# Performance work log

Hardware: AMD Instinct MI355X
Metric: run time of the kernel (lower is better)

The kernel has to match this reference:

```python
import jax, jax.numpy as jnp
import numpy as np

B, N, M = 8192, 64, 32          # batch, num_fields, embedding_dim
D = N * (N - 1) // 2            # 2016 pairwise-interaction rows of theta
OUT = 1024                      # block_out_dim
BN_EPS = 1e-5


def setup_inputs() -> dict:
    key = jax.random.key(0)
    k0, k1, k2, k3 = jax.random.split(key, 4)
    inputs = jax.random.normal(k0, (B, N * M), dtype=jnp.float32)
    W_z = jax.random.normal(k1, (N, N, M), dtype=jnp.float32) * 0.05
    theta = jax.random.normal(k2, (D, N), dtype=jnp.float32) * 0.05
    w_affine = jax.random.normal(k3, (OUT, N + D), dtype=jnp.float32) * 0.02
    b_affine = jnp.zeros((OUT,), dtype=jnp.float32)
    gamma = jnp.ones((OUT,), dtype=jnp.float32)
    beta = jnp.zeros((OUT,), dtype=jnp.float32)
    return {"inputs": inputs, "W_z": W_z, "theta": theta,
            "w_affine": w_affine, "b_affine": b_affine,
            "gamma": gamma, "beta": beta}


def reference(inputs, W_z, theta, w_affine, b_affine, gamma, beta):
    b = inputs.shape[0]
    x = inputs.reshape(b, N, M)                      # [B, N, M]
    # lz term: full quadratic form with W_z
    lz = jnp.einsum('bnm,dnm->bd', x, W_z)           # [B, N]
    # lp term: algebraically identical to einsum('bdnm,bdnm->bd') over
    # delta = einsum('bnm,dn->bdnm'): lp[b,d] = sum_n theta[d,n]^2 * sum_m x[b,n,m]^2
    x_sq = jnp.sum(x * x, axis=-1)                   # [B, N]
    lp = x_sq @ (theta * theta).T                    # [B, D]
    out = jnp.concatenate([lz, lp], axis=1)          # [B, N+D]
    out = out @ w_affine.T + b_affine                # [B, OUT]
    # BatchNorm1d in training mode (batch statistics, biased variance)
    mean = jnp.mean(out, axis=0)
    var = jnp.var(out, axis=0)
    out = (out - mean) * jax.lax.rsqrt(var + BN_EPS) * gamma + beta
    return out
```

## Files before the change

### kernel.cpp

```cpp
#include <hip/hip_runtime.h>
#include <stdint.h>

#define NROWS 8192
#define KX    2048
#define KA    2112
#define NF    64
#define DD    2016
#define WCOLS 2080
#define ODIM  1024
#define BN_EPS 1e-5f

#define A1_OT 32
#define A2_DC 8
#define A2_DPC 252
#define A2_OT 16

#define CONV_RPB 4
#define CONV_NB  (NROWS / CONV_RPB)
#define RED_NB   (ODIM * NF / 256)

#define A1A2_A1N 256
#define A1A2_TOT 768

#define NT (KA / 32)

using f32x4  = __attribute__((ext_vector_type(4))) float;
using bf16x8 = __attribute__((ext_vector_type(8))) short;

__device__ __forceinline__ short f2bf(float x) {
    uint32_t u = __float_as_uint(x);
    uint32_t r = (u + 0x7FFFu + ((u >> 16) & 1u)) >> 16;
    return (short)r;
}

__device__ __forceinline__ void gload16(const void* g, void* l) {
    __builtin_amdgcn_global_load_lds(
        (const __attribute__((address_space(1))) uint32_t*)g,
        (__attribute__((address_space(3))) uint32_t*)l, 16, 0, 0);
}

#define MFMA_BF16 __builtin_amdgcn_mfma_f32_16x16x32_bf16

__global__ __launch_bounds__(256) void conv_kern(const float* __restrict__ X,
                                                 short* __restrict__ Xa,
                                                 const float* __restrict__ partials,
                                                 short* __restrict__ Aw) {
    const int t = threadIdx.x;
    const int b = blockIdx.x;
    if (b < CONV_NB) {
#pragma unroll
        for (int r = 0; r < CONV_RPB; ++r) {
            const int row = b * CONV_RPB + r;
            const float4* xr = reinterpret_cast<const float4*>(X + (size_t)row * KX);
            float4 v0 = xr[t * 2];
            float4 v1 = xr[t * 2 + 1];
            bf16x8 s;
            s[0] = f2bf(v0.x); s[1] = f2bf(v0.y); s[2] = f2bf(v0.z); s[3] = f2bf(v0.w);
            s[4] = f2bf(v1.x); s[5] = f2bf(v1.y); s[6] = f2bf(v1.z); s[7] = f2bf(v1.w);
            short* outr = Xa + (size_t)row * KA;
            reinterpret_cast<bf16x8*>(outr)[t] = s;
            float sq = v0.x*v0.x + v0.y*v0.y + v0.z*v0.z + v0.w*v0.w
                     + v1.x*v1.x + v1.y*v1.y + v1.z*v1.z + v1.w*v1.w;
            sq += __shfl_xor(sq, 1);
            sq += __shfl_xor(sq, 2);
            if ((t & 3) == 0) outr[KX + (t >> 2)] = f2bf(sq - 32.0f);
        }
    } else {
        const int idx = (b - CONV_NB) * 256 + t;
        const int o = idx >> 6, n = idx & 63;
        float s = 0.f;
#pragma unroll
        for (int c = 0; c < A2_DC; ++c)
            s += partials[((size_t)c * ODIM + o) * NF + n];
        Aw[(size_t)o * KA + KX + n] = f2bf(s);
    }
}

__global__ __launch_bounds__(256) void a1a2_kern(short* __restrict__ Aw,
                                                 const float* __restrict__ Wa,
                                                 const float* __restrict__ Wz,
                                                 const float* __restrict__ theta,
                                                 float* __restrict__ partials) {
    const int bid = blockIdx.x;
    const int t = threadIdx.x;
    __shared__ __align__(16) float smem[4096];

    if (bid < A1A2_A1N) {
        const int k = (bid & 7) * 256 + t;
        const int o0 = (bid >> 3) * A1_OT;
        for (int idx = t; idx < A1_OT * 64; idx += 256)
            smem[idx] = Wa[(size_t)(o0 + (idx >> 6)) * WCOLS + (idx & 63)];
        float wz[64];
#pragma unroll
        for (int d = 0; d < 64; ++d) wz[d] = Wz[(size_t)d * KX + k];
        __syncthreads();
#pragma unroll 2
        for (int j = 0; j < A1_OT; ++j) {
            const float* war = &smem[j * 64];
            float acc = 0.f;
#pragma unroll
            for (int d = 0; d < 64; ++d) acc += war[d] * wz[d];
            Aw[(size_t)(o0 + j) * KA + k] = f2bf(acc);
        }
    } else {
        const int b = bid - A1A2_A1N;
        const int n = t & 63;
        const int g = t >> 6;
        const int chunk = b & 7;
        const int o0 = (b >> 3) * A2_OT;
        const int d0 = chunk * A2_DPC;
        float* waT = smem;
        for (int idx = t; idx < A2_OT * A2_DPC; idx += 256) {
            const int j = idx / A2_DPC, dd = idx - j * A2_DPC;
            waT[idx] = Wa[(size_t)(o0 + j) * WCOLS + NF + d0 + dd];
        }
        __syncthreads();
        float acc[A2_OT];
#pragma unroll
        for (int j = 0; j < A2_OT; ++j) acc[j] = 0.f;
        for (int i = g; i < A2_DPC; i += 4) {
            float th = theta[(size_t)(d0 + i) * NF + n];
            float th2 = th * th;
#pragma unroll
            for (int j = 0; j < A2_OT; ++j)
                acc[j] += waT[j * A2_DPC + i] * th2;
        }
        __syncthreads();
        float* red = smem;
#pragma unroll
        for (int j = 0; j < A2_OT; ++j) red[(g * A2_OT + j) * 64 + n] = acc[j];
        __syncthreads();
#pragma unroll
        for (int k2 = 0; k2 < A2_OT * 64 / 256; ++k2) {
            const int idx = t + k2 * 256;
            const int ol = idx >> 6, nn = idx & 63;
            float s = red[(0 * A2_OT + ol) * 64 + nn] + red[(1 * A2_OT + ol) * 64 + nn]
                    + red[(2 * A2_OT + ol) * 64 + nn] + red[(3 * A2_OT + ol) * 64 + nn];
            partials[((size_t)chunk * ODIM + o0 + ol) * NF + nn] = s;
        }
    }
}

__global__ __launch_bounds__(256) void gemm_kern(const short* __restrict__ Xa,
                                                 const short* __restrict__ Aw,
                                                 float* __restrict__ C,
                                                 float* __restrict__ sums) {
    __shared__ __align__(16) short As[3][128 * 32];
    __shared__ __align__(16) short Bs[3][128 * 32];
    const int tid  = threadIdx.x;
    const int lane = tid & 63;
    const int wid  = tid >> 6;
    const int wr = wid >> 1, wc = wid & 1;
    const int bm = blockIdx.x * 128;
    const int bn = blockIdx.y * 128;

    f32x4 acc[4][4] = {};

    const int c0 = tid, c1 = tid + 256;
    const int r0 = c0 >> 2, q0 = (c0 & 3) ^ ((r0 >> 1) & 3);
    const int r1 = c1 >> 2, q1 = (c1 & 3) ^ ((r1 >> 1) & 3);
    const short* gA0 = Xa + (size_t)(bm + r0) * KA + q0 * 8;
    const short* gA1 = Xa + (size_t)(bm + r1) * KA + q1 * 8;
    const short* gB0 = Aw + (size_t)(bn + r0) * KA + q0 * 8;
    const short* gB1 = Aw + (size_t)(bn + r1) * KA + q1 * 8;
    const int l0 = c0 * 8, l1 = c1 * 8;

    const int lq = lane >> 4;
    int offA[4], offB[4];
#pragma unroll
    for (int m = 0; m < 4; ++m) {
        int ra = wr * 64 + m * 16 + (lane & 15);
        offA[m] = ra * 32 + (lq ^ ((ra >> 1) & 3)) * 8;
        int rb = wc * 64 + m * 16 + (lane & 15);
        offB[m] = rb * 32 + (lq ^ ((rb >> 1) & 3)) * 8;
    }

#define STAGE(buf, kt) do {                         \
        const int ko_ = (kt) * 32;                  \
        gload16(gA0 + ko_, &As[buf][l0]);           \
        gload16(gA1 + ko_, &As[buf][l1]);           \
        gload16(gB0 + ko_, &Bs[buf][l0]);           \
        gload16(gB1 + ko_, &Bs[buf][l1]);           \
    } while (0)

#define TILE(cbuf, sbuf, kt) do {                                          \
        if ((kt) + 2 < NT) STAGE(sbuf, (kt) + 2);                          \
        bf16x8 a_[4], b_[4];                                               \
        _Pragma("unroll")                                                  \
        for (int m = 0; m < 4; ++m)                                        \
            a_[m] = *reinterpret_cast<const bf16x8*>(&As[cbuf][offA[m]]);  \
        _Pragma("unroll")                                                  \
        for (int n = 0; n < 4; ++n)                                        \
            b_[n] = *reinterpret_cast<const bf16x8*>(&Bs[cbuf][offB[n]]);  \
        asm volatile("s_waitcnt lgkmcnt(0)" ::: "memory");                 \
        __builtin_amdgcn_sched_barrier(0);                                 \
        _Pragma("unroll")                                                  \
        for (int m = 0; m < 4; ++m)                                        \
            _Pragma("unroll")                                              \
            for (int n = 0; n < 4; ++n)                                    \
                acc[m][n] = MFMA_BF16(a_[m], b_[n], acc[m][n], 0, 0, 0);   \
        if ((kt) + 2 < NT)                                                 \
            asm volatile("s_waitcnt vmcnt(4)" ::: "memory");               \
        else if ((kt) + 1 < NT)                                            \
            asm volatile("s_waitcnt vmcnt(0)" ::: "memory");               \
        __builtin_amdgcn_s_barrier();                                      \
    } while (0)

    STAGE(0, 0);
    STAGE(1, 1);
    asm volatile("s_waitcnt vmcnt(4)" ::: "memory");
    __builtin_amdgcn_s_barrier();

    for (int kt = 0; kt < NT; kt += 3) {
        TILE(0, 2, kt);
        TILE(1, 0, kt + 1);
        TILE(2, 1, kt + 2);
    }
#undef TILE
#undef STAGE

    const int rlo = (lane >> 4) * 4;
    const int cl  = lane & 15;
#pragma unroll
    for (int n = 0; n < 4; ++n) {
        const int col = bn + wc * 64 + n * 16 + cl;
        float s = 0.f, q = 0.f;
#pragma unroll
        for (int m = 0; m < 4; ++m) {
            const int rowb = bm + wr * 64 + m * 16 + rlo;
#pragma unroll
            for (int r2 = 0; r2 < 4; ++r2) {
                float v = acc[m][n][r2];
                C[(size_t)(rowb + r2) * ODIM + col] = v;
                s += v; q += v * v;
            }
        }
        s += __shfl_xor(s, 16); s += __shfl_xor(s, 32);
        q += __shfl_xor(q, 16); q += __shfl_xor(q, 32);
        if (lane < 16) {
            atomicAdd(&sums[col], s);
            atomicAdd(&sums[ODIM + col], q);
        }
    }
}

__global__ __launch_bounds__(256) void bn_apply(float* __restrict__ C,
                                                const float* __restrict__ sums,
                                                const float* __restrict__ gamma,
                                                const float* __restrict__ beta) {
    const int g = blockIdx.x * 256 + threadIdx.x;
    const int c4 = g & (ODIM / 4 - 1);
    const int row0 = g >> 8;
    const float inv = 1.0f / (float)NROWS;
    float4 sc, sh;
    {
        float4 s0 = reinterpret_cast<const float4*>(sums)[c4];
        float4 q0 = reinterpret_cast<const float4*>(sums + ODIM)[c4];
        float4 gm = reinterpret_cast<const float4*>(gamma)[c4];
        float4 bt = reinterpret_cast<const float4*>(beta)[c4];
        float m, v;
        m = s0.x * inv; v = q0.x * inv - m * m; sc.x = gm.x * rsqrtf(v + BN_EPS); sh.x = bt.x - m * sc.x;
        m = s0.y * inv; v = q0.y * inv - m * m; sc.y = gm.y * rsqrtf(v + BN_EPS); sh.y = bt.y - m * sc.y;
        m = s0.z * inv; v = q0.z * inv - m * m; sc.z = gm.z * rsqrtf(v + BN_EPS); sh.z = bt.z - m * sc.z;
        m = s0.w * inv; v = q0.w * inv - m * m; sc.w = gm.w * rsqrtf(v + BN_EPS); sh.w = bt.w - m * sc.w;
    }
#pragma unroll
    for (int r = 0; r < 4; ++r) {
        const size_t i = (size_t)(row0 + r * 2048) * (ODIM / 4) + c4;
        float4 v = reinterpret_cast<const float4*>(C)[i];
        v.x = v.x * sc.x + sh.x;
        v.y = v.y * sc.y + sh.y;
        v.z = v.z * sc.z + sh.z;
        v.w = v.w * sc.w + sh.w;
        reinterpret_cast<float4*>(C)[i] = v;
    }
}

extern "C" void kernel_launch(void* const* d_in, const int* in_sizes, int n_in,
                              void* d_out, int out_size, void* d_ws, size_t ws_size,
                              hipStream_t stream) {
    const float* X     = (const float*)d_in[0];
    const float* Wz    = (const float*)d_in[1];
    const float* theta = (const float*)d_in[2];
    const float* Wa    = (const float*)d_in[3];
    const float* gamma = (const float*)d_in[5];
    const float* beta  = (const float*)d_in[6];
    float* out = (float*)d_out;

    char* ws = (char*)d_ws;
    float* sums = (float*)ws;
    short* Xa = (short*)(ws + 16384);
    short* Aw = (short*)(ws + 16384 + (size_t)NROWS * KA * 2);
    float* partials = (float*)(ws + 16384 + (size_t)NROWS * KA * 2
                                        + (size_t)ODIM * KA * 2);

    hipMemsetAsync(sums, 0, 2 * ODIM * sizeof(float), stream);
    a1a2_kern<<<A1A2_TOT, 256, 0, stream>>>(Aw, Wa, Wz, theta, partials);
    conv_kern<<<CONV_NB + RED_NB, 256, 0, stream>>>(X, Xa, partials, Aw);
    gemm_kern<<<dim3(NROWS / 128, ODIM / 128), 256, 0, stream>>>(Xa, Aw, out, sums);
    bn_apply<<<NROWS / 4 * ODIM / 4 / 256, 256, 0, stream>>>(out, sums, gamma, beta);
}
```

Before: 114.8 us.

## Shrink GEMM tile to 64x128 with two waves and fold sums memset into prep kernel

The GEMM block tile drops from 128x128 with four waves to 64x128 with two waves, each wave still computing a 64x64 sub-tile. Staging loads and wait counts are adjusted to match. This doubles the grid to 1024 blocks, giving more blocks per CU and better load balance on the 256-CU part. The cost is lower reuse of the A/B tiles per block, so more global and L2 traffic. Separately, the memset of the BN sums buffer is removed and the zeroing is done by extra blocks in the a1a2 kernel, saving one launch.

```diff
diff --git a/kernel.cpp b/kernel.cpp
--- a/kernel.cpp
+++ b/kernel.cpp
@@ -20,8 +20,11 @@
 #define RED_NB   (ODIM * NF / 256)
 
 #define A1A2_A1N 256
-#define A1A2_TOT 768
-
+#define A1A2_A2E 768
+#define A1A2_TOT 776
+
+#define GBM 64
+#define GBN 128
 #define NT (KA / 32)
 
 using f32x4  = __attribute__((ext_vector_type(4))) float;
@@ -80,11 +83,16 @@
                                                  const float* __restrict__ Wa,
                                                  const float* __restrict__ Wz,
                                                  const float* __restrict__ theta,
-                                                 float* __restrict__ partials) {
+                                                 float* __restrict__ partials,
+                                                 float* __restrict__ sums) {
     const int bid = blockIdx.x;
     const int t = threadIdx.x;
     __shared__ __align__(16) float smem[4096];
 
+    if (bid >= A1A2_A2E) {
+        sums[(bid - A1A2_A2E) * 256 + t] = 0.f;
+        return;
+    }
     if (bid < A1A2_A1N) {
         const int k = (bid & 7) * 256 + t;
         const int o0 = (bid >> 3) * A1_OT;
@@ -141,35 +149,42 @@
     }
 }
 
-__global__ __launch_bounds__(256) void gemm_kern(const short* __restrict__ Xa,
+__global__ __launch_bounds__(128) void gemm_kern(const short* __restrict__ Xa,
                                                  const short* __restrict__ Aw,
                                                  float* __restrict__ C,
                                                  float* __restrict__ sums) {
-    __shared__ __align__(16) short As[3][128 * 32];
-    __shared__ __align__(16) short Bs[3][128 * 32];
+    __shared__ __align__(16) short As[3][GBM * 32];
+    __shared__ __align__(16) short Bs[3][GBN * 32];
     const int tid  = threadIdx.x;
     const int lane = tid & 63;
-    const int wid  = tid >> 6;
-    const int wr = wid >> 1, wc = wid & 1;
-    const int bm = blockIdx.x * 128;
-    const int bn = blockIdx.y * 128;
+    const int wc   = tid >> 6;
+    const int bm = blockIdx.x * GBM;
+    const int bn = blockIdx.y * GBN;
 
     f32x4 acc[4][4] = {};
 
-    const int c0 = tid, c1 = tid + 256;
-    const int r0 = c0 >> 2, q0 = (c0 & 3) ^ ((r0 >> 1) & 3);
-    const int r1 = c1 >> 2, q1 = (c1 & 3) ^ ((r1 >> 1) & 3);
-    const short* gA0 = Xa + (size_t)(bm + r0) * KA + q0 * 8;
-    const short* gA1 = Xa + (size_t)(bm + r1) * KA + q1 * 8;
-    const short* gB0 = Aw + (size_t)(bn + r0) * KA + q0 * 8;
-    const short* gB1 = Aw + (size_t)(bn + r1) * KA + q1 * 8;
-    const int l0 = c0 * 8, l1 = c1 * 8;
+    const short* gA[2]; int lA[2];
+#pragma unroll
+    for (int i = 0; i < 2; ++i) {
+        const int c = tid + i * 128;
+        const int r = c >> 2, q = (c & 3) ^ ((r >> 1) & 3);
+        gA[i] = Xa + (size_t)(bm + r) * KA + q * 8;
+        lA[i] = c * 8;
+    }
+    const short* gB[4]; int lB[4];
+#pragma unroll
+    for (int i = 0; i < 4; ++i) {
+        const int c = tid + i * 128;
+        const int r = c >> 2, q = (c & 3) ^ ((r >> 1) & 3);
+        gB[i] = Aw + (size_t)(bn + r) * KA + q * 8;
+        lB[i] = c * 8;
+    }
 
     const int lq = lane >> 4;
     int offA[4], offB[4];
 #pragma unroll
     for (int m = 0; m < 4; ++m) {
-        int ra = wr * 64 + m * 16 + (lane & 15);
+        int ra = m * 16 + (lane & 15);
         offA[m] = ra * 32 + (lq ^ ((ra >> 1) & 3)) * 8;
         int rb = wc * 64 + m * 16 + (lane & 15);
         offB[m] = rb * 32 + (lq ^ ((rb >> 1) & 3)) * 8;
@@ -177,10 +192,12 @@
 
 #define STAGE(buf, kt) do {                         \
         const int ko_ = (kt) * 32;                  \
-        gload16(gA0 + ko_, &As[buf][l0]);           \
-        gload16(gA1 + ko_, &As[buf][l1]);           \
-        gload16(gB0 + ko_, &Bs[buf][l0]);           \
-        gload16(gB1 + ko_, &Bs[buf][l1]);           \
+        gload16(gA[0] + ko_, &As[buf][lA[0]]);      \
+        gload16(gA[1] + ko_, &As[buf][lA[1]]);      \
+        gload16(gB[0] + ko_, &Bs[buf][lB[0]]);      \
+        gload16(gB[1] + ko_, &Bs[buf][lB[1]]);      \
+        gload16(gB[2] + ko_, &Bs[buf][lB[2]]);      \
+        gload16(gB[3] + ko_, &Bs[buf][lB[3]]);      \
     } while (0)
 
 #define TILE(cbuf, sbuf, kt) do {                                          \
@@ -200,7 +217,7 @@
             for (int n = 0; n < 4; ++n)                                    \
                 acc[m][n] = MFMA_BF16(a_[m], b_[n], acc[m][n], 0, 0, 0);   \
         if ((kt) + 2 < NT)                                                 \
-            asm volatile("s_waitcnt vmcnt(4)" ::: "memory");               \
+            asm volatile("s_waitcnt vmcnt(6)" ::: "memory");               \
         else if ((kt) + 1 < NT)                                            \
             asm volatile("s_waitcnt vmcnt(0)" ::: "memory");               \
         __builtin_amdgcn_s_barrier();                                      \
@@ -208,7 +225,7 @@
 
     STAGE(0, 0);
     STAGE(1, 1);
-    asm volatile("s_waitcnt vmcnt(4)" ::: "memory");
+    asm volatile("s_waitcnt vmcnt(6)" ::: "memory");
     __builtin_amdgcn_s_barrier();
 
     for (int kt = 0; kt < NT; kt += 3) {
@@ -227,7 +244,7 @@
         float s = 0.f, q = 0.f;
 #pragma unroll
         for (int m = 0; m < 4; ++m) {
-            const int rowb = bm + wr * 64 + m * 16 + rlo;
+            const int rowb = bm + m * 16 + rlo;
 #pragma unroll
             for (int r2 = 0; r2 < 4; ++r2) {
                 float v = acc[m][n][r2];
@@ -294,9 +311,8 @@
     float* partials = (float*)(ws + 16384 + (size_t)NROWS * KA * 2
                                         + (size_t)ODIM * KA * 2);
 
-    hipMemsetAsync(sums, 0, 2 * ODIM * sizeof(float), stream);
-    a1a2_kern<<<A1A2_TOT, 256, 0, stream>>>(Aw, Wa, Wz, theta, partials);
+    a1a2_kern<<<A1A2_TOT, 256, 0, stream>>>(Aw, Wa, Wz, theta, partials, sums);
     conv_kern<<<CONV_NB + RED_NB, 256, 0, stream>>>(X, Xa, partials, Aw);
-    gemm_kern<<<dim3(NROWS / 128, ODIM / 128), 256, 0, stream>>>(Xa, Aw, out, sums);
+    gemm_kern<<<dim3(NROWS / GBM, ODIM / GBN), 128, 0, stream>>>(Xa, Aw, out, sums);
     bn_apply<<<NROWS / 4 * ODIM / 4 / 256, 256, 0, stream>>>(out, sums, gamma, beta);
 }
```

After: 116.4 us. No clear change (+1.4%).
